# Performance work log

Hardware: AMD Instinct MI355X
Metric: run time of the kernel (lower is better)

## Reference

```python
import jax, jax.numpy as jnp
import numpy as np

N_NODES = 50000
N_EDGES = 800000
IN_CH = 128
HID_CH = 8
OUT_CH = 64
HEADS = 32
NEG_SLOPE = 0.2  # PyG GATConv default


def setup_inputs() -> dict:
    key = jax.random.key(0)
    ks = jax.random.split(key, 12)
    x = jax.random.normal(ks[0], (N_NODES, IN_CH), dtype=jnp.float32)
    # edge_index with no self loops (src != dst), matching PyG's remove_self_loops
    src = jax.random.randint(ks[1], (N_EDGES,), 0, N_NODES)
    off = jax.random.randint(ks[2], (N_EDGES,), 1, N_NODES)
    dst = (src + off) % N_NODES
    edge_index = jnp.stack([src, dst]).astype(jnp.int64)
    s = 0.1
    W1 = jax.random.normal(ks[3], (IN_CH, HEADS * HID_CH), dtype=jnp.float32) * s
    att_src1 = jax.random.normal(ks[4], (HEADS, HID_CH), dtype=jnp.float32) * s
    att_dst1 = jax.random.normal(ks[5], (HEADS, HID_CH), dtype=jnp.float32) * s
    b1 = jnp.zeros((HEADS * HID_CH,), dtype=jnp.float32)
    W2 = jax.random.normal(ks[6], (HEADS * HID_CH, OUT_CH), dtype=jnp.float32) * s
    att_src2 = jax.random.normal(ks[7], (1, OUT_CH), dtype=jnp.float32) * s
    att_dst2 = jax.random.normal(ks[8], (1, OUT_CH), dtype=jnp.float32) * s
    b2 = jnp.zeros((OUT_CH,), dtype=jnp.float32)
    return {"x": x, "edge_index": edge_index, "W1": W1, "att_src1": att_src1,
            "att_dst1": att_dst1, "b1": b1, "W2": W2, "att_src2": att_src2,
            "att_dst2": att_dst2, "b2": b2}


def _gat_conv(x, src, dst, W, a_src, a_dst, bias, concat):
    # Faithful PyG GATConv: linear -> per-edge LeakyReLU score -> segment softmax over dst -> scatter-add
    n = x.shape[0]
    H, C = a_src.shape
    h = (x @ W).reshape(n, H, C)                      # [N,H,C]
    alpha_src = jnp.sum(h * a_src, axis=-1)           # [N,H]
    alpha_dst = jnp.sum(h * a_dst, axis=-1)           # [N,H]
    e = jax.nn.leaky_relu(alpha_src[src] + alpha_dst[dst], negative_slope=NEG_SLOPE)  # [E,H]
    e_max = jax.ops.segment_max(e, dst, num_segments=n)          # every node has a self loop
    ex = jnp.exp(e - e_max[dst])
    denom = jax.ops.segment_sum(ex, dst, num_segments=n)
    alpha = ex / (denom[dst] + 1e-16)                 # [E,H]
    msg = h[src] * alpha[:, :, None]                  # [E,H,C]
    out = jax.ops.segment_sum(msg, dst, num_segments=n)          # [N,H,C]
    out = out.reshape(n, H * C) if concat else out.mean(axis=1)
    return out + bias


def reference(x, edge_index, W1, att_src1, att_dst1, b1, W2, att_src2, att_dst2, b2):
    n = x.shape[0]
    loops = jnp.arange(n, dtype=edge_index.dtype)
    src = jnp.concatenate([edge_index[0], loops])     # add_self_loops (PyG default)
    dst = jnp.concatenate([edge_index[1], loops])
    h = _gat_conv(x, src, dst, W1, att_src1, att_dst1, b1, concat=True)
    h = _gat_conv(h, src, dst, W2, att_src2, att_dst2, b2, concat=False)
    return jax.nn.sigmoid(h)
```

## Files before the change

kernel.cpp:

```cpp
#include <hip/hip_runtime.h>
#include <hip/hip_bf16.h>

constexpr int N  = 50000;
constexpr int E  = 800000;
constexpr int F0 = 128;
constexpr int H1 = 32;
constexpr int F1 = 256;
constexpr int F2 = 64;
constexpr int NB = (N + 255) / 256;
constexpr int NPAD = 782 * 64;
constexpr int W1SZ = F0 * F1;
constexpr int W2SZ = F1 * F2;
constexpr int VA1SZ = 64 * F0;
constexpr int VA2SZ = 16 * F1;
constexpr float NEG_SLOPE = 0.2f;

typedef unsigned short u16;
typedef unsigned int   u32;
typedef __attribute__((ext_vector_type(8))) short bf16x8;
typedef __attribute__((ext_vector_type(4))) float f32x4;

__device__ __forceinline__ float leaky(float e) {
    return fmaxf(e, 0.f) + NEG_SLOPE * fminf(e, 0.f);
}
__device__ __forceinline__ u16 f2bf(float f) {
    u32 u = __builtin_bit_cast(u32, f);
    u += 0x7fffu + ((u >> 16) & 1u);
    return (u16)(u >> 16);
}
__device__ __forceinline__ u32 pack2(float a, float b) {
    return (u32)f2bf(a) | ((u32)f2bf(b) << 16);
}
__device__ __forceinline__ void up2(u32 v, float& lo, float& hi) {
    lo = __builtin_bit_cast(float, v << 16);
    hi = __builtin_bit_cast(float, v & 0xffff0000u);
}

__device__ __forceinline__ int is64_check(const void* ei) {
    const unsigned long long* p = (const unsigned long long*)ei;
    unsigned long long v = p[threadIdx.x & 63];
    return __all(v < (unsigned long long)N) ? 1 : 0;
}
__device__ __forceinline__ int load_idx(const void* ei, long long i, int is64) {
    return is64 ? (int)((const long long*)ei)[i] : ((const int*)ei)[i];
}

__global__ void k_count(const void* __restrict__ ei, int* __restrict__ deg) {
    int is64 = is64_check(ei);
    int e = blockIdx.x * blockDim.x + threadIdx.x;
    if (e >= E) return;
    int dst = load_idx(ei, (long long)E + e, is64);
    atomicAdd(&deg[dst], 1);
}
__global__ __launch_bounds__(256) void k_bsum(const int* __restrict__ deg, int* __restrict__ bsum) {
    int b = blockIdx.x, t = threadIdx.x, i = b * 256 + t;
    int v = (i < N) ? deg[i] : 0;
#pragma unroll
    for (int o = 1; o < 64; o <<= 1) v += __shfl_xor(v, o, 64);
    __shared__ int sw[4];
    if ((t & 63) == 0) sw[t >> 6] = v;
    __syncthreads();
    if (t == 0) bsum[b] = sw[0] + sw[1] + sw[2] + sw[3];
}
__global__ __launch_bounds__(256) void k_bscan(int* __restrict__ bsum, int* __restrict__ rsN) {
    int t = threadIdx.x, lane = t & 63, wy = t >> 6;
    int v = (t < NB) ? bsum[t] : 0;
    int inc = v;
#pragma unroll
    for (int o = 1; o < 64; o <<= 1) { int u = __shfl_up(inc, o, 64); if (lane >= o) inc += u; }
    __shared__ int wtot[4];
    if (lane == 63) wtot[wy] = inc;
    __syncthreads();
    int offs = 0;
    for (int k = 0; k < wy; k++) offs += wtot[k];
    int excl = offs + inc - v;
    if (t < NB) bsum[t] = excl;
    if (t == NB - 1) *rsN = excl + v;
}
__global__ __launch_bounds__(256) void k_rs(const int* __restrict__ deg,
                                            const int* __restrict__ bsum, int* __restrict__ rs) {
    int b = blockIdx.x, t = threadIdx.x, i = b * 256 + t;
    int lane = t & 63, wy = t >> 6;
    int v = (i < N) ? deg[i] : 0;
    int inc = v;
#pragma unroll
    for (int o = 1; o < 64; o <<= 1) { int u = __shfl_up(inc, o, 64); if (lane >= o) inc += u; }
    __shared__ int wtot[4];
    if (lane == 63) wtot[wy] = inc;
    __syncthreads();
    int offs = bsum[b];
    for (int k = 0; k < wy; k++) offs += wtot[k];
    if (i < N) rs[i] = offs + inc - v;
}
__global__ void k_scatter(const void* __restrict__ ei,
                          int* __restrict__ rs2, int* __restrict__ csr) {
    int is64 = is64_check(ei);
    int e = blockIdx.x * blockDim.x + threadIdx.x;
    if (e >= E) return;
    int src = load_idx(ei, e, is64);
    int dst = load_idx(ei, (long long)E + e, is64);
    int pos = atomicAdd(&rs2[dst], 1);
    csr[pos] = src;
}

__global__ __launch_bounds__(256) void k_prepw(
        const float* __restrict__ W1, const float* __restrict__ W2,
        const float* __restrict__ as1, const float* __restrict__ ad1,
        const float* __restrict__ a2s, const float* __restrict__ a2d,
        u16* __restrict__ w1t, u16* __restrict__ w2t,
        u16* __restrict__ va1t, u16* __restrict__ va2t) {
    int i = blockIdx.x * 256 + threadIdx.x;
    if (i < W1SZ) {
        int n = i >> 7, k = i & 127;
        w1t[(n << 7) + (k ^ ((n & 7) << 3))] = f2bf(W1[k * F1 + n]);
    } else if (i < W1SZ + W2SZ) {
        int j = i - W1SZ;
        int n = j >> 8, k = j & 255;
        w2t[(n << 8) + (k ^ ((n & 7) << 3))] = f2bf(W2[k * F2 + n]);
    } else if (i < W1SZ + W2SZ + VA1SZ) {
        int j = i - W1SZ - W2SZ;
        int c = j >> 7, k = j & 127;
        const float* a = (c < 32) ? as1 : ad1;
        int h = c & 31;
        float s = 0.f;
#pragma unroll
        for (int cc = 0; cc < 8; cc++) s += W1[k * F1 + h * 8 + cc] * a[h * 8 + cc];
        va1t[(c << 7) + (k ^ ((c & 7) << 3))] = f2bf(s);
    } else if (i < W1SZ + W2SZ + VA1SZ + VA2SZ) {
        int j = i - W1SZ - W2SZ - VA1SZ;
        int jj = j >> 8, k = j & 255;
        float s = 0.f;
        if (jj < 2) {
            const float* a = jj ? a2d : a2s;
            for (int c = 0; c < 64; c++) s += W2[k * F2 + c] * a[c];
        }
        va2t[(jj << 8) + (k ^ ((jj & 7) << 3))] = f2bf(s);
    }
}

__global__ __launch_bounds__(256) void k_gemm1(
        const float* __restrict__ x, const u16* __restrict__ w1t,
        const u16* __restrict__ va1t, u16* __restrict__ h1b,
        float* __restrict__ asrc1, float* __restrict__ adst1) {
    __shared__ u16 As[64 * 128];
    int r0 = blockIdx.x * 64;
    int t = threadIdx.x, w = t >> 6, l = t & 63;
    {
        int r = t >> 2, k0 = (t & 3) * 32, rr = r0 + r;
        int swz = (r & 7) << 3;
        float4 f[8];
        if (rr < N) {
            const float4* px = (const float4*)(x + (size_t)rr * F0 + k0);
#pragma unroll
            for (int j = 0; j < 8; j++) f[j] = px[j];
        } else {
#pragma unroll
            for (int j = 0; j < 8; j++) f[j] = make_float4(0.f, 0.f, 0.f, 0.f);
        }
#pragma unroll
        for (int g = 0; g < 4; g++) {
            uint4 st;
            st.x = pack2(f[2 * g].x, f[2 * g].y);
            st.y = pack2(f[2 * g].z, f[2 * g].w);
            st.z = pack2(f[2 * g + 1].x, f[2 * g + 1].y);
            st.w = pack2(f[2 * g + 1].z, f[2 * g + 1].w);
            *(uint4*)(As + r * 128 + ((k0 + 8 * g) ^ swz)) = st;
        }
    }
    bf16x8 bfrag[4][4];
#pragma unroll
    for (int n = 0; n < 4; n++) {
        int col = w * 64 + n * 16 + (l & 15);
        const u16* wrow = w1t + col * 128;
        int swz = (col & 7) << 3;
#pragma unroll
        for (int ks = 0; ks < 4; ks++)
            bfrag[n][ks] = *(const bf16x8*)(wrow + ((ks * 32 + (l >> 4) * 8) ^ swz));
    }
    __syncthreads();
    f32x4 z = {0.f, 0.f, 0.f, 0.f};
    f32x4 acc[4][4], acc5[4];
#pragma unroll
    for (int m = 0; m < 4; m++) {
        acc5[m] = z;
#pragma unroll
        for (int n = 0; n < 4; n++) acc[m][n] = z;
    }
    int c5 = w * 16 + (l & 15);
    const u16* varow = va1t + c5 * 128;
    int swz5 = (c5 & 7) << 3;
#pragma unroll
    for (int ks = 0; ks < 4; ks++) {
        bf16x8 b5 = *(const bf16x8*)(varow + ((ks * 32 + (l >> 4) * 8) ^ swz5));
#pragma unroll
        for (int m = 0; m < 4; m++) {
            int row = m * 16 + (l & 15);
            bf16x8 a = *(const bf16x8*)(As + row * 128 +
                                        ((ks * 32 + (l >> 4) * 8) ^ ((row & 7) << 3)));
#pragma unroll
            for (int n = 0; n < 4; n++)
                acc[m][n] = __builtin_amdgcn_mfma_f32_16x16x32_bf16(a, bfrag[n][ks], acc[m][n], 0, 0, 0);
            acc5[m] = __builtin_amdgcn_mfma_f32_16x16x32_bf16(a, b5, acc5[m], 0, 0, 0);
        }
    }
#pragma unroll
    for (int m = 0; m < 4; m++) {
        int rbase = r0 + m * 16 + (l >> 4) * 4;
#pragma unroll
        for (int n = 0; n < 4; n++) {
            int col = w * 64 + n * 16 + (l & 15);
#pragma unroll
            for (int r = 0; r < 4; r++) {
                int rr = rbase + r;
                if (rr < N) h1b[(size_t)rr * 256 + (col ^ ((rr & 7) << 3))] = f2bf(acc[m][n][r]);
            }
        }
#pragma unroll
        for (int r = 0; r < 4; r++) {
            int rr = rbase + r;
            if (rr < N) {
                float v = acc5[m][r];
                if (c5 < 32) asrc1[(size_t)rr * H1 + c5] = v;
                else         adst1[(size_t)rr * H1 + (c5 - 32)] = v;
            }
        }
    }
}

__global__ __launch_bounds__(256) void k_edge1(
        const int* __restrict__ rs, const int* __restrict__ csr,
        const u16* __restrict__ h1b, const float* __restrict__ asrc,
        const float* __restrict__ adst, const float* __restrict__ b1,
        u16* __restrict__ outb) {
    int d = blockIdx.x * 4 + (threadIdx.x >> 6);
    if (d >= N) return;
    int l = threadIdx.x & 63;
    int half = l >> 5, h = l & 31;
    int beg = rs[d], end = rs[d + 1];
    float adh = adst[(size_t)d * H1 + h];
    float wself = __expf(leaky(asrc[(size_t)d * H1 + h] + adh));
    float w0 = half ? 0.f : wself;
    float den = w0;
    float c0, c1, c2, c3, c4, c5, c6, c7;
    {
        uint4 vd = *(const uint4*)(h1b + (size_t)d * 256 + 8 * (h ^ (d & 7)));
        float t0, t1;
        up2(vd.x, t0, t1); c0 = w0 * t0; c1 = w0 * t1;
        up2(vd.y, t0, t1); c2 = w0 * t0; c3 = w0 * t1;
        up2(vd.z, t0, t1); c4 = w0 * t0; c5 = w0 * t1;
        up2(vd.w, t0, t1); c6 = w0 * t0; c7 = w0 * t1;
    }
    const uint4 z4 = {0u, 0u, 0u, 0u};
    for (int i0 = beg; i0 < end; i0 += 16) {
        int   s[8];
        float av[8];
        uint4 v[8];
#pragma unroll
        for (int k = 0; k < 8; k++) {
            int i = i0 + 2 * k + half;
            s[k] = (i < end) ? csr[i] : -1;
        }
#pragma unroll
        for (int k = 0; k < 8; k++) {
            av[k] = 0.f; v[k] = z4;
            if (s[k] >= 0) {
                av[k] = asrc[(size_t)s[k] * H1 + h];
                v[k] = *(const uint4*)(h1b + (size_t)s[k] * 256 + 8 * (h ^ (s[k] & 7)));
            }
        }
#pragma unroll
        for (int k = 0; k < 8; k++) {
            float wv = (s[k] >= 0) ? __expf(leaky(av[k] + adh)) : 0.f;
            den += wv;
            float t0, t1;
            up2(v[k].x, t0, t1); c0 = fmaf(wv, t0, c0); c1 = fmaf(wv, t1, c1);
            up2(v[k].y, t0, t1); c2 = fmaf(wv, t0, c2); c3 = fmaf(wv, t1, c3);
            up2(v[k].z, t0, t1); c4 = fmaf(wv, t0, c4); c5 = fmaf(wv, t1, c5);
            up2(v[k].w, t0, t1); c6 = fmaf(wv, t0, c6); c7 = fmaf(wv, t1, c7);
        }
    }
    den += __shfl_xor(den, 32, 64);
    c0 += __shfl_xor(c0, 32, 64); c1 += __shfl_xor(c1, 32, 64);
    c2 += __shfl_xor(c2, 32, 64); c3 += __shfl_xor(c3, 32, 64);
    c4 += __shfl_xor(c4, 32, 64); c5 += __shfl_xor(c5, 32, 64);
    c6 += __shfl_xor(c6, 32, 64); c7 += __shfl_xor(c7, 32, 64);
    if (!half) {
        float inv = 1.f / (den + 1e-16f);
        int ch = 8 * h;
        uint4 st;
        st.x = pack2(c0 * inv + b1[ch],     c1 * inv + b1[ch + 1]);
        st.y = pack2(c2 * inv + b1[ch + 2], c3 * inv + b1[ch + 3]);
        st.z = pack2(c4 * inv + b1[ch + 4], c5 * inv + b1[ch + 5]);
        st.w = pack2(c6 * inv + b1[ch + 6], c7 * inv + b1[ch + 7]);
        *(uint4*)(outb + (size_t)d * 256 + 8 * (h ^ (d & 7))) = st;
    }
}

__global__ __launch_bounds__(256) void k_gemm2(
        const u16* __restrict__ ab, const u16* __restrict__ w2t,
        const u16* __restrict__ va2t, u16* __restrict__ h2b,
        float* __restrict__ asrc2, float* __restrict__ adst2) {
    __shared__ u16 As[64 * 256];
    int r0 = blockIdx.x * 64;
    int t = threadIdx.x, w = t >> 6, l = t & 63;
    {
        const uint4* gsrc = (const uint4*)(ab + (size_t)r0 * 256);
        uint4* lds = (uint4*)As;
        for (int i = t; i < 2048; i += 256) lds[i] = gsrc[i];
    }
    __syncthreads();
    f32x4 z = {0.f, 0.f, 0.f, 0.f};
    f32x4 acc[4], acc5 = z;
#pragma unroll
    for (int n = 0; n < 4; n++) acc[n] = z;
    int row = w * 16 + (l & 15);
    int swzA = (row & 7) << 3;
    int j5 = l & 15;
    int swz5 = (j5 & 7) << 3;
#pragma unroll
    for (int ks = 0; ks < 8; ks++) {
        int ka = ks * 32 + (l >> 4) * 8;
        bf16x8 a = *(const bf16x8*)(As + row * 256 + (ka ^ swzA));
#pragma unroll
        for (int n = 0; n < 4; n++) {
            int col = n * 16 + (l & 15);
            bf16x8 b = *(const bf16x8*)(w2t + col * 256 + (ka ^ ((col & 7) << 3)));
            acc[n] = __builtin_amdgcn_mfma_f32_16x16x32_bf16(a, b, acc[n], 0, 0, 0);
        }
        bf16x8 b5 = *(const bf16x8*)(va2t + j5 * 256 + (ka ^ swz5));
        acc5 = __builtin_amdgcn_mfma_f32_16x16x32_bf16(a, b5, acc5, 0, 0, 0);
    }
#pragma unroll
    for (int n = 0; n < 4; n++) {
        int col = n * 16 + (l & 15);
#pragma unroll
        for (int r = 0; r < 4; r++) {
            int rr = r0 + w * 16 + (l >> 4) * 4 + r;
            if (rr < N) h2b[(size_t)rr * F2 + col] = f2bf(acc[n][r]);
        }
    }
#pragma unroll
    for (int r = 0; r < 4; r++) {
        int rr = r0 + w * 16 + (l >> 4) * 4 + r;
        if (rr < N) {
            if (j5 == 0) asrc2[rr] = acc5[r];
            else if (j5 == 1) adst2[rr] = acc5[r];
        }
    }
}

__global__ __launch_bounds__(256) void k_edge2(
        const int* __restrict__ rs, const int* __restrict__ csr,
        const u16* __restrict__ h2b, const float* __restrict__ asrc,
        const float* __restrict__ adst, const float* __restrict__ b2,
        float* __restrict__ out) {
    int d = blockIdx.x * 4 + (threadIdx.x >> 6);
    if (d >= N) return;
    int l = threadIdx.x & 63;
    int q = l >> 3, c8 = (l & 7) * 8;
    int beg = rs[d], end = rs[d + 1];
    float add_ = adst[d];
    float wself = __expf(leaky(asrc[d] + add_));
    float w0 = (q == 0) ? wself : 0.f;
    float den = w0;
    float c0, c1, c2, c3, c4, c5, c6, c7;
    {
        uint4 vd = *(const uint4*)(h2b + (size_t)d * F2 + c8);
        float t0, t1;
        up2(vd.x, t0, t1); c0 = w0 * t0; c1 = w0 * t1;
        up2(vd.y, t0, t1); c2 = w0 * t0; c3 = w0 * t1;
        up2(vd.z, t0, t1); c4 = w0 * t0; c5 = w0 * t1;
        up2(vd.w, t0, t1); c6 = w0 * t0; c7 = w0 * t1;
    }
    const uint4 z4 = {0u, 0u, 0u, 0u};
    for (int i0 = beg; i0 < end; i0 += 16) {
        int   s[2];
        float av[2];
        uint4 v[2];
#pragma unroll
        for (int k = 0; k < 2; k++) {
            int i = i0 + 8 * k + q;
            s[k] = (i < end) ? csr[i] : -1;
        }
#pragma unroll
        for (int k = 0; k < 2; k++) {
            av[k] = 0.f; v[k] = z4;
            if (s[k] >= 0) {
                av[k] = asrc[s[k]];
                v[k] = *(const uint4*)(h2b + (size_t)s[k] * F2 + c8);
            }
        }
#pragma unroll
        for (int k = 0; k < 2; k++) {
            float wv = (s[k] >= 0) ? __expf(leaky(av[k] + add_)) : 0.f;
            den += wv;
            float t0, t1;
            up2(v[k].x, t0, t1); c0 = fmaf(wv, t0, c0); c1 = fmaf(wv, t1, c1);
            up2(v[k].y, t0, t1); c2 = fmaf(wv, t0, c2); c3 = fmaf(wv, t1, c3);
            up2(v[k].z, t0, t1); c4 = fmaf(wv, t0, c4); c5 = fmaf(wv, t1, c5);
            up2(v[k].w, t0, t1); c6 = fmaf(wv, t0, c6); c7 = fmaf(wv, t1, c7);
        }
    }
#pragma unroll
    for (int o = 8; o < 64; o <<= 1) {
        den += __shfl_xor(den, o, 64);
        c0 += __shfl_xor(c0, o, 64); c1 += __shfl_xor(c1, o, 64);
        c2 += __shfl_xor(c2, o, 64); c3 += __shfl_xor(c3, o, 64);
        c4 += __shfl_xor(c4, o, 64); c5 += __shfl_xor(c5, o, 64);
        c6 += __shfl_xor(c6, o, 64); c7 += __shfl_xor(c7, o, 64);
    }
    if (q == 0) {
        float inv = 1.f / (den + 1e-16f);
        float4 o1, o2;
        o1.x = 1.f / (1.f + __expf(-(c0 * inv + b2[c8])));
        o1.y = 1.f / (1.f + __expf(-(c1 * inv + b2[c8 + 1])));
        o1.z = 1.f / (1.f + __expf(-(c2 * inv + b2[c8 + 2])));
        o1.w = 1.f / (1.f + __expf(-(c3 * inv + b2[c8 + 3])));
        o2.x = 1.f / (1.f + __expf(-(c4 * inv + b2[c8 + 4])));
        o2.y = 1.f / (1.f + __expf(-(c5 * inv + b2[c8 + 5])));
        o2.z = 1.f / (1.f + __expf(-(c6 * inv + b2[c8 + 6])));
        o2.w = 1.f / (1.f + __expf(-(c7 * inv + b2[c8 + 7])));
        *(float4*)(out + (size_t)d * F2 + c8) = o1;
        *(float4*)(out + (size_t)d * F2 + c8 + 4) = o2;
    }
}

extern "C" void kernel_launch(void* const* d_in, const int* in_sizes, int n_in,
                              void* d_out, int out_size, void* d_ws, size_t ws_size,
                              hipStream_t stream) {
    const float* x   = (const float*)d_in[0];
    const void*  ei  = d_in[1];
    const float* W1  = (const float*)d_in[2];
    const float* as1 = (const float*)d_in[3];
    const float* ad1 = (const float*)d_in[4];
    const float* b1  = (const float*)d_in[5];
    const float* W2  = (const float*)d_in[6];
    const float* a2s = (const float*)d_in[7];
    const float* a2d = (const float*)d_in[8];
    const float* b2  = (const float*)d_in[9];
    float* out = (float*)d_out;

    char* wp = (char*)d_ws;
    size_t off = 0;
    auto alloc = [&](size_t bytes) {
        void* p = wp + off;
        off = (off + bytes + 255) & ~(size_t)255;
        return p;
    };
    int* deg   = (int*)alloc((size_t)N * 4);
    int* rs    = (int*)alloc((size_t)(N + 1) * 4);
    int* rs2   = (int*)alloc((size_t)N * 4);
    int* bsum  = (int*)alloc((size_t)NB * 4);
    int* csr   = (int*)alloc((size_t)E * 4);
    u16* w1t   = (u16*)alloc((size_t)W1SZ * 2);
    u16* w2t   = (u16*)alloc((size_t)W2SZ * 2);
    u16* va1t  = (u16*)alloc((size_t)VA1SZ * 2);
    u16* va2t  = (u16*)alloc((size_t)VA2SZ * 2);
    u16* h1b   = (u16*)alloc((size_t)NPAD * F1 * 2);
    u16* h1ab  = (u16*)alloc((size_t)NPAD * F1 * 2);
    u16* h2b   = (u16*)alloc((size_t)NPAD * F2 * 2);
    float* asrc1 = (float*)alloc((size_t)N * H1 * 4);
    float* adst1 = (float*)alloc((size_t)N * H1 * 4);
    float* asrc2 = (float*)alloc((size_t)N * 4);
    float* adst2 = (float*)alloc((size_t)N * 4);

    hipMemsetAsync(deg, 0, (size_t)N * 4, stream);

    k_count<<<(E + 255) / 256, 256, 0, stream>>>(ei, deg);
    k_bsum<<<NB, 256, 0, stream>>>(deg, bsum);
    k_bscan<<<1, 256, 0, stream>>>(bsum, rs + N);
    k_rs<<<NB, 256, 0, stream>>>(deg, bsum, rs);
    hipMemcpyAsync(rs2, rs, (size_t)N * 4, hipMemcpyDeviceToDevice, stream);
    k_scatter<<<(E + 255) / 256, 256, 0, stream>>>(ei, rs2, csr);

    k_prepw<<<(W1SZ + W2SZ + VA1SZ + VA2SZ + 255) / 256, 256, 0, stream>>>(
        W1, W2, as1, ad1, a2s, a2d, w1t, w2t, va1t, va2t);
    k_gemm1<<<NPAD / 64, 256, 0, stream>>>(x, w1t, va1t, h1b, asrc1, adst1);
    k_edge1<<<(N + 3) / 4, 256, 0, stream>>>(rs, csr, h1b, asrc1, adst1, b1, h1ab);
    k_gemm2<<<NPAD / 64, 256, 0, stream>>>(h1ab, w2t, va2t, h2b, asrc2, adst2);
    k_edge2<<<(N + 3) / 4, 256, 0, stream>>>(rs, csr, h2b, asrc2, adst2, b2, out);
}
```

Baseline: 248.7 us.

## Merge setup kernels, store layer-1 attention logits as bf16, use packed FMA

Folds the degree memset into the weight-prep kernel and the edge-count pass into gemm1 as extra blocks, and makes k_rs write rs2 directly so the device-to-device memcpy goes away. Together these cut the number of launches and let independent work share a grid. Layer-1 per-node attention logits are now stored as bf16 instead of fp32, halving the gather traffic in edge1 at some cost in precision. The edge accumulators switch to float2 vectors with elementwise fma, aiming for packed FMA instructions.

```diff
diff --git a/kernel.cpp b/kernel.cpp
--- a/kernel.cpp
+++ b/kernel.cpp
@@ -13,15 +13,24 @@
 constexpr int W2SZ = F1 * F2;
 constexpr int VA1SZ = 64 * F0;
 constexpr int VA2SZ = 16 * F1;
+constexpr int PREPB = (W1SZ + W2SZ + VA1SZ + VA2SZ) / 256;
+constexpr int INITB = PREPB + NB;
+constexpr int GB1 = NPAD / 64;
+constexpr int CB  = (E + 255) / 256;
 constexpr float NEG_SLOPE = 0.2f;
 
 typedef unsigned short u16;
 typedef unsigned int   u32;
 typedef __attribute__((ext_vector_type(8))) short bf16x8;
 typedef __attribute__((ext_vector_type(4))) float f32x4;
+typedef __attribute__((ext_vector_type(2))) float f32x2;
 
 __device__ __forceinline__ float leaky(float e) {
     return fmaxf(e, 0.f) + NEG_SLOPE * fminf(e, 0.f);
+}
+__device__ __forceinline__ float bf2f(u16 u) {
+    u32 v = ((u32)u) << 16;
+    return __builtin_bit_cast(float, v);
 }
 __device__ __forceinline__ u16 f2bf(float f) {
     u32 u = __builtin_bit_cast(u32, f);
@@ -35,6 +44,12 @@
     lo = __builtin_bit_cast(float, v << 16);
     hi = __builtin_bit_cast(float, v & 0xffff0000u);
 }
+__device__ __forceinline__ f32x2 up2v(u32 v) {
+    f32x2 r;
+    r.x = __builtin_bit_cast(float, v << 16);
+    r.y = __builtin_bit_cast(float, v & 0xffff0000u);
+    return r;
+}
 
 __device__ __forceinline__ int is64_check(const void* ei) {
     const unsigned long long* p = (const unsigned long long*)ei;
@@ -45,71 +60,19 @@
     return is64 ? (int)((const long long*)ei)[i] : ((const int*)ei)[i];
 }
 
-__global__ void k_count(const void* __restrict__ ei, int* __restrict__ deg) {
-    int is64 = is64_check(ei);
-    int e = blockIdx.x * blockDim.x + threadIdx.x;
-    if (e >= E) return;
-    int dst = load_idx(ei, (long long)E + e, is64);
-    atomicAdd(&deg[dst], 1);
-}
-__global__ __launch_bounds__(256) void k_bsum(const int* __restrict__ deg, int* __restrict__ bsum) {
-    int b = blockIdx.x, t = threadIdx.x, i = b * 256 + t;
-    int v = (i < N) ? deg[i] : 0;
-#pragma unroll
-    for (int o = 1; o < 64; o <<= 1) v += __shfl_xor(v, o, 64);
-    __shared__ int sw[4];
-    if ((t & 63) == 0) sw[t >> 6] = v;
-    __syncthreads();
-    if (t == 0) bsum[b] = sw[0] + sw[1] + sw[2] + sw[3];
-}
-__global__ __launch_bounds__(256) void k_bscan(int* __restrict__ bsum, int* __restrict__ rsN) {
-    int t = threadIdx.x, lane = t & 63, wy = t >> 6;
-    int v = (t < NB) ? bsum[t] : 0;
-    int inc = v;
-#pragma unroll
-    for (int o = 1; o < 64; o <<= 1) { int u = __shfl_up(inc, o, 64); if (lane >= o) inc += u; }
-    __shared__ int wtot[4];
-    if (lane == 63) wtot[wy] = inc;
-    __syncthreads();
-    int offs = 0;
-    for (int k = 0; k < wy; k++) offs += wtot[k];
-    int excl = offs + inc - v;
-    if (t < NB) bsum[t] = excl;
-    if (t == NB - 1) *rsN = excl + v;
-}
-__global__ __launch_bounds__(256) void k_rs(const int* __restrict__ deg,
-                                            const int* __restrict__ bsum, int* __restrict__ rs) {
-    int b = blockIdx.x, t = threadIdx.x, i = b * 256 + t;
-    int lane = t & 63, wy = t >> 6;
-    int v = (i < N) ? deg[i] : 0;
-    int inc = v;
-#pragma unroll
-    for (int o = 1; o < 64; o <<= 1) { int u = __shfl_up(inc, o, 64); if (lane >= o) inc += u; }
-    __shared__ int wtot[4];
-    if (lane == 63) wtot[wy] = inc;
-    __syncthreads();
-    int offs = bsum[b];
-    for (int k = 0; k < wy; k++) offs += wtot[k];
-    if (i < N) rs[i] = offs + inc - v;
-}
-__global__ void k_scatter(const void* __restrict__ ei,
-                          int* __restrict__ rs2, int* __restrict__ csr) {
-    int is64 = is64_check(ei);
-    int e = blockIdx.x * blockDim.x + threadIdx.x;
-    if (e >= E) return;
-    int src = load_idx(ei, e, is64);
-    int dst = load_idx(ei, (long long)E + e, is64);
-    int pos = atomicAdd(&rs2[dst], 1);
-    csr[pos] = src;
-}
-
-__global__ __launch_bounds__(256) void k_prepw(
+__global__ __launch_bounds__(256) void k_init(
         const float* __restrict__ W1, const float* __restrict__ W2,
         const float* __restrict__ as1, const float* __restrict__ ad1,
         const float* __restrict__ a2s, const float* __restrict__ a2d,
         u16* __restrict__ w1t, u16* __restrict__ w2t,
-        u16* __restrict__ va1t, u16* __restrict__ va2t) {
-    int i = blockIdx.x * 256 + threadIdx.x;
+        u16* __restrict__ va1t, u16* __restrict__ va2t, int* __restrict__ deg) {
+    int b = blockIdx.x;
+    if (b >= PREPB) {
+        int i = (b - PREPB) * 256 + threadIdx.x;
+        if (i < N) deg[i] = 0;
+        return;
+    }
+    int i = b * 256 + threadIdx.x;
     if (i < W1SZ) {
         int n = i >> 7, k = i & 127;
         w1t[(n << 7) + (k ^ ((n & 7) << 3))] = f2bf(W1[k * F1 + n]);
@@ -138,10 +101,20 @@
     }
 }
 
-__global__ __launch_bounds__(256) void k_gemm1(
+__global__ __launch_bounds__(256) void k_gemm1count(
         const float* __restrict__ x, const u16* __restrict__ w1t,
         const u16* __restrict__ va1t, u16* __restrict__ h1b,
-        float* __restrict__ asrc1, float* __restrict__ adst1) {
+        u16* __restrict__ asrc1b, u16* __restrict__ adst1b,
+        const void* __restrict__ ei, int* __restrict__ deg) {
+    if (blockIdx.x >= GB1) {
+        int is64 = is64_check(ei);
+        int e = (blockIdx.x - GB1) * 256 + threadIdx.x;
+        if (e < E) {
+            int dst = load_idx(ei, (long long)E + e, is64);
+            atomicAdd(&deg[dst], 1);
+        }
+        return;
+    }
     __shared__ u16 As[64 * 128];
     int r0 = blockIdx.x * 64;
     int t = threadIdx.x, w = t >> 6, l = t & 63;
@@ -219,42 +192,95 @@
         for (int r = 0; r < 4; r++) {
             int rr = rbase + r;
             if (rr < N) {
-                float v = acc5[m][r];
-                if (c5 < 32) asrc1[(size_t)rr * H1 + c5] = v;
-                else         adst1[(size_t)rr * H1 + (c5 - 32)] = v;
+                u16 v = f2bf(acc5[m][r]);
+                if (c5 < 32) asrc1b[(size_t)rr * H1 + c5] = v;
+                else         adst1b[(size_t)rr * H1 + (c5 - 32)] = v;
             }
         }
     }
+}
+
+__global__ __launch_bounds__(256) void k_bsum(const int* __restrict__ deg, int* __restrict__ bsum) {
+    int b = blockIdx.x, t = threadIdx.x, i = b * 256 + t;
+    int v = (i < N) ? deg[i] : 0;
+#pragma unroll
+    for (int o = 1; o < 64; o <<= 1) v += __shfl_xor(v, o, 64);
+    __shared__ int sw[4];
+    if ((t & 63) == 0) sw[t >> 6] = v;
+    __syncthreads();
+    if (t == 0) bsum[b] = sw[0] + sw[1] + sw[2] + sw[3];
+}
+__global__ __launch_bounds__(256) void k_bscan(int* __restrict__ bsum, int* __restrict__ rsN) {
+    int t = threadIdx.x, lane = t & 63, wy = t >> 6;
+    int v = (t < NB) ? bsum[t] : 0;
+    int inc = v;
+#pragma unroll
+    for (int o = 1; o < 64; o <<= 1) { int u = __shfl_up(inc, o, 64); if (lane >= o) inc += u; }
+    __shared__ int wtot[4];
+    if (lane == 63) wtot[wy] = inc;
+    __syncthreads();
+    int offs = 0;
+    for (int k = 0; k < wy; k++) offs += wtot[k];
+    int excl = offs + inc - v;
+    if (t < NB) bsum[t] = excl;
+    if (t == NB - 1) *rsN = excl + v;
+}
+__global__ __launch_bounds__(256) void k_rs(const int* __restrict__ deg,
+                                            const int* __restrict__ bsum,
+                                            int* __restrict__ rs, int* __restrict__ rs2) {
+    int b = blockIdx.x, t = threadIdx.x, i = b * 256 + t;
+    int lane = t & 63, wy = t >> 6;
+    int v = (i < N) ? deg[i] : 0;
+    int inc = v;
+#pragma unroll
+    for (int o = 1; o < 64; o <<= 1) { int u = __shfl_up(inc, o, 64); if (lane >= o) inc += u; }
+    __shared__ int wtot[4];
+    if (lane == 63) wtot[wy] = inc;
+    __syncthreads();
+    int offs = bsum[b];
+    for (int k = 0; k < wy; k++) offs += wtot[k];
+    if (i < N) {
+        int e = offs + inc - v;
+        rs[i] = e;
+        rs2[i] = e;
+    }
+}
+__global__ void k_scatter(const void* __restrict__ ei,
+                          int* __restrict__ rs2, int* __restrict__ csr) {
+    int is64 = is64_check(ei);
+    int e = blockIdx.x * blockDim.x + threadIdx.x;
+    if (e >= E) return;
+    int src = load_idx(ei, e, is64);
+    int dst = load_idx(ei, (long long)E + e, is64);
+    int pos = atomicAdd(&rs2[dst], 1);
+    csr[pos] = src;
 }
 
 __global__ __launch_bounds__(256) void k_edge1(
         const int* __restrict__ rs, const int* __restrict__ csr,
-        const u16* __restrict__ h1b, const float* __restrict__ asrc,
-        const float* __restrict__ adst, const float* __restrict__ b1,
+        const u16* __restrict__ h1b, const u16* __restrict__ asrcb,
+        const u16* __restrict__ adstb, const float* __restrict__ b1,
         u16* __restrict__ outb) {
     int d = blockIdx.x * 4 + (threadIdx.x >> 6);
     if (d >= N) return;
     int l = threadIdx.x & 63;
     int half = l >> 5, h = l & 31;
     int beg = rs[d], end = rs[d + 1];
-    float adh = adst[(size_t)d * H1 + h];
-    float wself = __expf(leaky(asrc[(size_t)d * H1 + h] + adh));
+    float adh = bf2f(adstb[(size_t)d * H1 + h]);
+    float wself = __expf(leaky(bf2f(asrcb[(size_t)d * H1 + h]) + adh));
     float w0 = half ? 0.f : wself;
     float den = w0;
-    float c0, c1, c2, c3, c4, c5, c6, c7;
+    f32x2 c0, c1, c2, c3;
     {
         uint4 vd = *(const uint4*)(h1b + (size_t)d * 256 + 8 * (h ^ (d & 7)));
-        float t0, t1;
-        up2(vd.x, t0, t1); c0 = w0 * t0; c1 = w0 * t1;
-        up2(vd.y, t0, t1); c2 = w0 * t0; c3 = w0 * t1;
-        up2(vd.z, t0, t1); c4 = w0 * t0; c5 = w0 * t1;
-        up2(vd.w, t0, t1); c6 = w0 * t0; c7 = w0 * t1;
+        c0 = up2v(vd.x) * w0;
+        c1 = up2v(vd.y) * w0;
+        c2 = up2v(vd.z) * w0;
+        c3 = up2v(vd.w) * w0;
     }
     const uint4 z4 = {0u, 0u, 0u, 0u};
     for (int i0 = beg; i0 < end; i0 += 16) {
-        int   s[8];
-        float av[8];
-        uint4 v[8];
+        int s[8]; u16 avu[8]; uint4 v[8];
 #pragma unroll
         for (int k = 0; k < 8; k++) {
             int i = i0 + 2 * k + half;
@@ -262,36 +288,36 @@
         }
 #pragma unroll
         for (int k = 0; k < 8; k++) {
-            av[k] = 0.f; v[k] = z4;
+            avu[k] = 0; v[k] = z4;
             if (s[k] >= 0) {
-                av[k] = asrc[(size_t)s[k] * H1 + h];
+                avu[k] = asrcb[(size_t)s[k] * H1 + h];
                 v[k] = *(const uint4*)(h1b + (size_t)s[k] * 256 + 8 * (h ^ (s[k] & 7)));
             }
         }
 #pragma unroll
         for (int k = 0; k < 8; k++) {
-            float wv = (s[k] >= 0) ? __expf(leaky(av[k] + adh)) : 0.f;
+            float wv = (s[k] >= 0) ? __expf(leaky(bf2f(avu[k]) + adh)) : 0.f;
             den += wv;
-            float t0, t1;
-            up2(v[k].x, t0, t1); c0 = fmaf(wv, t0, c0); c1 = fmaf(wv, t1, c1);
-            up2(v[k].y, t0, t1); c2 = fmaf(wv, t0, c2); c3 = fmaf(wv, t1, c3);
-            up2(v[k].z, t0, t1); c4 = fmaf(wv, t0, c4); c5 = fmaf(wv, t1, c5);
-            up2(v[k].w, t0, t1); c6 = fmaf(wv, t0, c6); c7 = fmaf(wv, t1, c7);
+            f32x2 w2v = {wv, wv};
+            c0 = __builtin_elementwise_fma(up2v(v[k].x), w2v, c0);
+            c1 = __builtin_elementwise_fma(up2v(v[k].y), w2v, c1);
+            c2 = __builtin_elementwise_fma(up2v(v[k].z), w2v, c2);
+            c3 = __builtin_elementwise_fma(up2v(v[k].w), w2v, c3);
         }
     }
     den += __shfl_xor(den, 32, 64);
-    c0 += __shfl_xor(c0, 32, 64); c1 += __shfl_xor(c1, 32, 64);
-    c2 += __shfl_xor(c2, 32, 64); c3 += __shfl_xor(c3, 32, 64);
-    c4 += __shfl_xor(c4, 32, 64); c5 += __shfl_xor(c5, 32, 64);
-    c6 += __shfl_xor(c6, 32, 64); c7 += __shfl_xor(c7, 32, 64);
+    c0.x += __shfl_xor(c0.x, 32, 64); c0.y += __shfl_xor(c0.y, 32, 64);
+    c1.x += __shfl_xor(c1.x, 32, 64); c1.y += __shfl_xor(c1.y, 32, 64);
+    c2.x += __shfl_xor(c2.x, 32, 64); c2.y += __shfl_xor(c2.y, 32, 64);
+    c3.x += __shfl_xor(c3.x, 32, 64); c3.y += __shfl_xor(c3.y, 32, 64);
     if (!half) {
         float inv = 1.f / (den + 1e-16f);
         int ch = 8 * h;
         uint4 st;
-        st.x = pack2(c0 * inv + b1[ch],     c1 * inv + b1[ch + 1]);
-        st.y = pack2(c2 * inv + b1[ch + 2], c3 * inv + b1[ch + 3]);
-        st.z = pack2(c4 * inv + b1[ch + 4], c5 * inv + b1[ch + 5]);
-        st.w = pack2(c6 * inv + b1[ch + 6], c7 * inv + b1[ch + 7]);
+        st.x = pack2(c0.x * inv + b1[ch],     c0.y * inv + b1[ch + 1]);
+        st.y = pack2(c1.x * inv + b1[ch + 2], c1.y * inv + b1[ch + 3]);
+        st.z = pack2(c2.x * inv + b1[ch + 4], c2.y * inv + b1[ch + 5]);
+        st.w = pack2(c3.x * inv + b1[ch + 6], c3.y * inv + b1[ch + 7]);
         *(uint4*)(outb + (size_t)d * 256 + 8 * (h ^ (d & 7))) = st;
     }
 }
@@ -363,20 +389,17 @@
     float wself = __expf(leaky(asrc[d] + add_));
     float w0 = (q == 0) ? wself : 0.f;
     float den = w0;
-    float c0, c1, c2, c3, c4, c5, c6, c7;
+    f32x2 c0, c1, c2, c3;
     {
         uint4 vd = *(const uint4*)(h2b + (size_t)d * F2 + c8);
-        float t0, t1;
-        up2(vd.x, t0, t1); c0 = w0 * t0; c1 = w0 * t1;
-        up2(vd.y, t0, t1); c2 = w0 * t0; c3 = w0 * t1;
-        up2(vd.z, t0, t1); c4 = w0 * t0; c5 = w0 * t1;
-        up2(vd.w, t0, t1); c6 = w0 * t0; c7 = w0 * t1;
+        c0 = up2v(vd.x) * w0;
+        c1 = up2v(vd.y) * w0;
+        c2 = up2v(vd.z) * w0;
+        c3 = up2v(vd.w) * w0;
     }
     const uint4 z4 = {0u, 0u, 0u, 0u};
     for (int i0 = beg; i0 < end; i0 += 16) {
-        int   s[2];
-        float av[2];
-        uint4 v[2];
+        int s[2]; float av[2]; uint4 v[2];
 #pragma unroll
         for (int k = 0; k < 2; k++) {
             int i = i0 + 8 * k + q;
@@ -394,32 +417,32 @@
         for (int k = 0; k < 2; k++) {
             float wv = (s[k] >= 0) ? __expf(leaky(av[k] + add_)) : 0.f;
             den += wv;
-            float t0, t1;
-            up2(v[k].x, t0, t1); c0 = fmaf(wv, t0, c0); c1 = fmaf(wv, t1, c1);
-            up2(v[k].y, t0, t1); c2 = fmaf(wv, t0, c2); c3 = fmaf(wv, t1, c3);
-            up2(v[k].z, t0, t1); c4 = fmaf(wv, t0, c4); c5 = fmaf(wv, t1, c5);
-            up2(v[k].w, t0, t1); c6 = fmaf(wv, t0, c6); c7 = fmaf(wv, t1, c7);
+            f32x2 w2v = {wv, wv};
+            c0 = __builtin_elementwise_fma(up2v(v[k].x), w2v, c0);
+            c1 = __builtin_elementwise_fma(up2v(v[k].y), w2v, c1);
+            c2 = __builtin_elementwise_fma(up2v(v[k].z), w2v, c2);
+            c3 = __builtin_elementwise_fma(up2v(v[k].w), w2v, c3);
         }
     }
 #pragma unroll
     for (int o = 8; o < 64; o <<= 1) {
         den += __shfl_xor(den, o, 64);
-        c0 += __shfl_xor(c0, o, 64); c1 += __shfl_xor(c1, o, 64);
-        c2 += __shfl_xor(c2, o, 64); c3 += __shfl_xor(c3, o, 64);
-        c4 += __shfl_xor(c4, o, 64); c5 += __shfl_xor(c5, o, 64);
-        c6 += __shfl_xor(c6, o, 64); c7 += __shfl_xor(c7, o, 64);
+        c0.x += __shfl_xor(c0.x, o, 64); c0.y += __shfl_xor(c0.y, o, 64);
+        c1.x += __shfl_xor(c1.x, o, 64); c1.y += __shfl_xor(c1.y, o, 64);
+        c2.x += __shfl_xor(c2.x, o, 64); c2.y += __shfl_xor(c2.y, o, 64);
+        c3.x += __shfl_xor(c3.x, o, 64); c3.y += __shfl_xor(c3.y, o, 64);
     }
     if (q == 0) {
         float inv = 1.f / (den + 1e-16f);
         float4 o1, o2;
-        o1.x = 1.f / (1.f + __expf(-(c0 * inv + b2[c8])));
-        o1.y = 1.f / (1.f + __expf(-(c1 * inv + b2[c8 + 1])));
-        o1.z = 1.f / (1.f + __expf(-(c2 * inv + b2[c8 + 2])));
-        o1.w = 1.f / (1.f + __expf(-(c3 * inv + b2[c8 + 3])));
-        o2.x = 1.f / (1.f + __expf(-(c4 * inv + b2[c8 + 4])));
-        o2.y = 1.f / (1.f + __expf(-(c5 * inv + b2[c8 + 5])));
-        o2.z = 1.f / (1.f + __expf(-(c6 * inv + b2[c8 + 6])));
-        o2.w = 1.f / (1.f + __expf(-(c7 * inv + b2[c8 + 7])));
+        o1.x = 1.f / (1.f + __expf(-(c0.x * inv + b2[c8])));
+        o1.y = 1.f / (1.f + __expf(-(c0.y * inv + b2[c8 + 1])));
+        o1.z = 1.f / (1.f + __expf(-(c1.x * inv + b2[c8 + 2])));
+        o1.w = 1.f / (1.f + __expf(-(c1.y * inv + b2[c8 + 3])));
+        o2.x = 1.f / (1.f + __expf(-(c2.x * inv + b2[c8 + 4])));
+        o2.y = 1.f / (1.f + __expf(-(c2.y * inv + b2[c8 + 5])));
+        o2.z = 1.f / (1.f + __expf(-(c3.x * inv + b2[c8 + 6])));
+        o2.w = 1.f / (1.f + __expf(-(c3.y * inv + b2[c8 + 7])));
         *(float4*)(out + (size_t)d * F2 + c8) = o1;
         *(float4*)(out + (size_t)d * F2 + c8 + 4) = o2;
     }
@@ -459,24 +482,20 @@
     u16* h1b   = (u16*)alloc((size_t)NPAD * F1 * 2);
     u16* h1ab  = (u16*)alloc((size_t)NPAD * F1 * 2);
     u16* h2b   = (u16*)alloc((size_t)NPAD * F2 * 2);
-    float* asrc1 = (float*)alloc((size_t)N * H1 * 4);
-    float* adst1 = (float*)alloc((size_t)N * H1 * 4);
+    u16* asrc1b = (u16*)alloc((size_t)N * H1 * 2);
+    u16* adst1b = (u16*)alloc((size_t)N * H1 * 2);
     float* asrc2 = (float*)alloc((size_t)N * 4);
     float* adst2 = (float*)alloc((size_t)N * 4);
 
-    hipMemsetAsync(deg, 0, (size_t)N * 4, stream);
-
-    k_count<<<(E + 255) / 256, 256, 0, stream>>>(ei, deg);
+    k_init<<<INITB, 256, 0, stream>>>(W1, W2, as1, ad1, a2s, a2d,
+                                      w1t, w2t, va1t, va2t, deg);
+    k_gemm1count<<<GB1 + CB, 256, 0, stream>>>(x, w1t, va1t, h1b,
+                                               asrc1b, adst1b, ei, deg);
     k_bsum<<<NB, 256, 0, stream>>>(deg, bsum);
     k_bscan<<<1, 256, 0, stream>>>(bsum, rs + N);
-    k_rs<<<NB, 256, 0, stream>>>(deg, bsum, rs);
-    hipMemcpyAsync(rs2, rs, (size_t)N * 4, hipMemcpyDeviceToDevice, stream);
-    k_scatter<<<(E + 255) / 256, 256, 0, stream>>>(ei, rs2, csr);
-
-    k_prepw<<<(W1SZ + W2SZ + VA1SZ + VA2SZ + 255) / 256, 256, 0, stream>>>(
-        W1, W2, as1, ad1, a2s, a2d, w1t, w2t, va1t, va2t);
-    k_gemm1<<<NPAD / 64, 256, 0, stream>>>(x, w1t, va1t, h1b, asrc1, adst1);
-    k_edge1<<<(N + 3) / 4, 256, 0, stream>>>(rs, csr, h1b, asrc1, adst1, b1, h1ab);
-    k_gemm2<<<NPAD / 64, 256, 0, stream>>>(h1ab, w2t, va2t, h2b, asrc2, adst2);
+    k_rs<<<NB, 256, 0, stream>>>(deg, bsum, rs, rs2);
+    k_scatter<<<CB, 256, 0, stream>>>(ei, rs2, csr);
+    k_edge1<<<(N + 3) / 4, 256, 0, stream>>>(rs, csr, h1b, asrc1b, adst1b, b1, h1ab);
+    k_gemm2<<<GB1, 256, 0, stream>>>(h1ab, w2t, va2t, h2b, asrc2, adst2);
     k_edge2<<<(N + 3) / 4, 256, 0, stream>>>(rs, csr, h2b, asrc2, adst2, b2, out);
 }
```

Result: faster. 231.4 us (-7.0%).
